# Kernel tuning notes

Measured on AMD Instinct MI355X. Metric: run time of the kernel, lower is better.

The kernel has to match this reference:

```python
import jax, jax.numpy as jnp
import numpy as np

WINDOW_SIZE = 5
CONSISTENCY_WEIGHT = 1.0


def _wsum(x, w):
    # sliding-window sum along axis 1 via exclusive cumsum differences
    s = jnp.cumsum(x, axis=1)
    s = jnp.pad(s, ((0, 0), (1, 0)))
    return s[:, w:] - s[:, :-w]  # [B, L-w+1]


def setup_inputs() -> dict:
    key = jax.random.key(0)
    k1, k2, k3 = jax.random.split(key, 3)
    B, L, C = 512, 16384, 2
    return {
        "predictions": jax.random.normal(k1, (B, L, C), dtype=jnp.float32),
        "targets": jax.random.randint(k2, (B, L), 0, 2, dtype=jnp.int32),
        "mask": jax.random.randint(k3, (B, L), 0, 2, dtype=jnp.int32),
    }


def reference(predictions, targets, mask):
    w = WINDOW_SIZE
    probs = jax.nn.softmax(predictions, axis=-1)[..., 1]  # [B, L]
    t = targets.astype(jnp.float32)
    m = mask.astype(jnp.float32)

    msum = _wsum(m, w)                       # [B, W]
    denom = jnp.maximum(msum, 1.0)           # clamp(min=1.0)
    spm = _wsum(probs * m, w)
    stm = _wsum(t * m, w)
    sp2m = _wsum(probs * probs * m, w)
    st2m = _wsum(t * t * m, w)

    pmean = spm / denom
    tmean = stm / denom
    # masked biased variance: sum((x - mean)^2 * m) / clamp(msum, 1)
    pvar = (sp2m - 2.0 * pmean * spm + pmean * pmean * msum) / denom
    tvar = (st2m - 2.0 * tmean * stm + tmean * tmean * msum) / denom

    mse = jnp.mean((pvar - tvar) ** 2, axis=0)          # per-window MSE over batch, [W]
    valid = (jnp.sum(msum, axis=0) > 0).astype(jnp.float32)  # skip windows with zero mask
    cnt = jnp.maximum(jnp.sum(valid), 1.0)
    loss = jnp.sum(mse * valid) / cnt * CONSISTENCY_WEIGHT
    return loss
```

## Files before the change

### kernel.cpp

```cpp
#include <hip/hip_runtime.h>
#include <math.h>

#define BATCH 512
#define LEN   16384
#define WIN   5
#define WOUT  (LEN - WIN + 1)
#define TPB   256
#define WPT   4
#define WPB   (TPB * WPT)
#define EPT   (WPT + WIN - 1)
#define NCH2  16

__device__ __forceinline__ float fast_rcp(float x) {
    float r = __builtin_amdgcn_rcpf(x);
    return r * fmaf(-x, r, 2.0f);
}

struct RowRaw {
    int4   m0, m1, t0, t1;
    float4 q0, q1, q2, q3;
};

struct RowArr {
    float m[EPT], tm[EPT], pm[EPT], p2m[EPT];
};

__device__ __forceinline__ RowRaw load_row(const float* __restrict__ pred,
                                           const int*   __restrict__ tgt,
                                           const int*   __restrict__ msk,
                                           size_t base) {
    RowRaw r;
    r.m0 = *(const int4*)(msk + base);
    r.m1 = *(const int4*)(msk + base + 4);
    r.t0 = *(const int4*)(tgt + base);
    r.t1 = *(const int4*)(tgt + base + 4);
    r.q0 = *(const float4*)(pred + base * 2);
    r.q1 = *(const float4*)(pred + base * 2 + 4);
    r.q2 = *(const float4*)(pred + base * 2 + 8);
    r.q3 = *(const float4*)(pred + base * 2 + 12);
    return r;
}

__device__ __forceinline__ RowArr convert_row(const RowRaw& r) {
    RowArr a;
    const int mi[EPT] = {r.m0.x, r.m0.y, r.m0.z, r.m0.w,
                         r.m1.x, r.m1.y, r.m1.z, r.m1.w};
    const int ti[EPT] = {r.t0.x, r.t0.y, r.t0.z, r.t0.w,
                         r.t1.x, r.t1.y, r.t1.z, r.t1.w};
    const float dx[EPT] = {r.q0.x - r.q0.y, r.q0.z - r.q0.w,
                           r.q1.x - r.q1.y, r.q1.z - r.q1.w,
                           r.q2.x - r.q2.y, r.q2.z - r.q2.w,
                           r.q3.x - r.q3.y, r.q3.z - r.q3.w};
#pragma unroll
    for (int i = 0; i < EPT; ++i) {
        const float p  = fast_rcp(1.0f + __expf(dx[i]));
        const float mf = (float)mi[i];
        a.m[i]   = mf;
        a.tm[i]  = (float)(ti[i] & mi[i]);
        a.pm[i]  = p * mf;
        a.p2m[i] = p * p * mf;
    }
    return a;
}

__device__ __forceinline__ void windows_row(const RowArr& a,
                                            float accd2[WPT], float accms[WPT]) {
#pragma unroll
    for (int w = 0; w < WPT; ++w) {
        float msum = 0.f, stm = 0.f, spm = 0.f, sp2m = 0.f;
#pragma unroll
        for (int k = 0; k < WIN; ++k) {
            msum += a.m[w + k];
            stm  += a.tm[w + k];
            spm  += a.pm[w + k];
            sp2m += a.p2m[w + k];
        }
        const float denom = fmaxf(msum, 1.0f);
        const float inv   = fast_rcp(denom);
        const float pmean = spm * inv;
        const float tmean = stm * inv;
        const float pvar  = (sp2m - 2.0f * pmean * spm + pmean * pmean * msum) * inv;
        const float tvar  = (stm  - 2.0f * tmean * stm + tmean * tmean * msum) * inv;
        const float d = pvar - tvar;
        accd2[w] += d * d;
        accms[w] += msum;
    }
}

__global__ __launch_bounds__(TPB)
void bcl_partial_kernel(const float* __restrict__ pred,
                        const int*   __restrict__ tgt,
                        const int*   __restrict__ msk,
                        float* __restrict__ part_d2,
                        float* __restrict__ part_ms,
                        int bper) {
    const int j0 = blockIdx.x * WPB + (int)threadIdx.x * WPT;
    if (j0 >= WOUT) return;
    const int b0 = blockIdx.y * bper;

    float accd2[WPT] = {0.f, 0.f, 0.f, 0.f};
    float accms[WPT] = {0.f, 0.f, 0.f, 0.f};

    size_t base = (size_t)b0 * LEN + j0;

    RowRaw raw = load_row(pred, tgt, msk, base);
    RowArr arr = convert_row(raw);

    for (int it = 1; it < bper; ++it) {
        raw = load_row(pred, tgt, msk, base + (size_t)it * LEN);
        windows_row(arr, accd2, accms);
        arr = convert_row(raw);
    }
    windows_row(arr, accd2, accms);

    *(float4*)(part_d2 + (size_t)blockIdx.y * WOUT + j0) =
        make_float4(accd2[0], accd2[1], accd2[2], accd2[3]);
    *(float4*)(part_ms + (size_t)blockIdx.y * WOUT + j0) =
        make_float4(accms[0], accms[1], accms[2], accms[3]);
}

__global__ __launch_bounds__(TPB)
void bcl_chunk_reduce(const float* __restrict__ part_d2,
                      const float* __restrict__ part_ms,
                      float* __restrict__ p2_d2,
                      float* __restrict__ p2_ms,
                      double* __restrict__ accum,
                      unsigned int* __restrict__ ticket,
                      int rf) {
    if (blockIdx.x == 0 && blockIdx.y == 0 && threadIdx.x == 0) {
        accum[0] = 0.0; accum[1] = 0.0; *ticket = 0u;
    }
    const int j = blockIdx.x * blockDim.x + threadIdx.x;
    if (j >= WOUT) return;
    const int c0 = blockIdx.y * rf;
    float d2 = 0.f, ms = 0.f;
#pragma unroll 8
    for (int c = c0; c < c0 + rf; ++c) {
        d2 += part_d2[(size_t)c * WOUT + j];
        ms += part_ms[(size_t)c * WOUT + j];
    }
    p2_d2[(size_t)blockIdx.y * WOUT + j] = d2;
    p2_ms[(size_t)blockIdx.y * WOUT + j] = ms;
}

__global__ __launch_bounds__(TPB)
void bcl_window_reduce(const float* __restrict__ p2_d2,
                       const float* __restrict__ p2_ms,
                       double* __restrict__ accum,
                       unsigned int* __restrict__ ticket,
                       float* __restrict__ out,
                       int nch2) {
    const int j = blockIdx.x * blockDim.x + threadIdx.x;
    double num = 0.0, cnt = 0.0;
    if (j < WOUT) {
        float d2 = 0.f, ms = 0.f;
#pragma unroll 8
        for (int c = 0; c < nch2; ++c) {
            d2 += p2_d2[(size_t)c * WOUT + j];
            ms += p2_ms[(size_t)c * WOUT + j];
        }
        if (ms > 0.f) {
            num = (double)d2 * (1.0 / (double)BATCH);
            cnt = 1.0;
        }
    }
    for (int off = 32; off > 0; off >>= 1) {
        num += __shfl_down(num, off, 64);
        cnt += __shfl_down(cnt, off, 64);
    }
    __shared__ double s_num[4], s_cnt[4];
    const int lane = threadIdx.x & 63, wave = threadIdx.x >> 6;
    if (lane == 0) { s_num[wave] = num; s_cnt[wave] = cnt; }
    __syncthreads();
    if (threadIdx.x == 0) {
        double n = 0.0, c = 0.0;
        const int nw = (int)(blockDim.x >> 6);
        for (int wv = 0; wv < nw; ++wv) { n += s_num[wv]; c += s_cnt[wv]; }
        atomicAdd(&accum[0], n);
        atomicAdd(&accum[1], c);
        __threadfence();
        const unsigned int t = atomicAdd(ticket, 1u);
        if (t == gridDim.x - 1) {
            out[0] = (float)(accum[0] / fmax(accum[1], 1.0));
        }
    }
}

extern "C" void kernel_launch(void* const* d_in, const int* in_sizes, int n_in,
                              void* d_out, int out_size, void* d_ws, size_t ws_size,
                              hipStream_t stream) {
    const float* pred = (const float*)d_in[0];
    const int*   tgt  = (const int*)d_in[1];
    const int*   msk  = (const int*)d_in[2];
    float* out = (float*)d_out;

    int nchunks = 128;
    while (nchunks > 2) {
        size_t need = (size_t)(nchunks + NCH2) * WOUT * 2 * sizeof(float) + 256;
        if (need <= ws_size) break;
        nchunks >>= 1;
    }
    const int bper = BATCH / nchunks;
    const int nch2 = (nchunks >= NCH2) ? NCH2 : nchunks;
    const int rf   = nchunks / nch2;

    float* part_d2 = (float*)d_ws;
    float* part_ms = part_d2 + (size_t)nchunks * WOUT;
    float* p2_d2   = part_ms + (size_t)nchunks * WOUT;
    float* p2_ms   = p2_d2   + (size_t)NCH2 * WOUT;
    size_t off = ((size_t)((char*)(p2_ms + (size_t)NCH2 * WOUT) - (char*)d_ws) + 15) & ~(size_t)15;
    double* accum = (double*)((char*)d_ws + off);
    unsigned int* ticket = (unsigned int*)(accum + 2);

    const int WBLKS = (WOUT + WPB - 1) / WPB;
    dim3 g1(WBLKS, nchunks);
    bcl_partial_kernel<<<g1, TPB, 0, stream>>>(pred, tgt, msk, part_d2, part_ms, bper);

    const int RBLKS = (WOUT + TPB - 1) / TPB;
    dim3 gA(RBLKS, nch2);
    bcl_chunk_reduce<<<gA, TPB, 0, stream>>>(part_d2, part_ms, p2_d2, p2_ms,
                                             accum, ticket, rf);

    bcl_window_reduce<<<RBLKS, TPB, 0, stream>>>(p2_d2, p2_ms, accum, ticket, out, nch2);
}
```

Baseline: 164.7 us.

## Fuse partial and reduction kernels into one cooperative launch with grid sync

Replaces the three-kernel pipeline with a single cooperative kernel that computes per-chunk partial window sums, grid-syncs, reduces over chunks and windows, then grid-syncs again to write the final loss. The chunk count drops from 128 to 64, so each block handles more batch rows, and the manual software prefetch of the next row is removed from the partial loop. The aim is to remove kernel-launch gaps and the intermediate second-level reduction. The trade-offs are grid.sync overhead, fewer blocks in flight, and a fallback path that runs if the cooperative launch fails.

```diff
diff --git a/kernel.cpp b/kernel.cpp
--- a/kernel.cpp
+++ b/kernel.cpp
@@ -1,5 +1,8 @@
 #include <hip/hip_runtime.h>
+#include <hip/hip_cooperative_groups.h>
 #include <math.h>
+
+namespace cg = cooperative_groups;
 
 #define BATCH 512
 #define LEN   16384
@@ -9,6 +12,8 @@
 #define WPT   4
 #define WPB   (TPB * WPT)
 #define EPT   (WPT + WIN - 1)
+#define WBLKS ((WOUT + WPB - 1) / WPB)
+#define RWGS  ((WOUT + TPB - 1) / TPB)
 #define NCH2  16
 
 __device__ __forceinline__ float fast_rcp(float x) {
@@ -20,7 +25,6 @@
     int4   m0, m1, t0, t1;
     float4 q0, q1, q2, q3;
 };
-
 struct RowArr {
     float m[EPT], tm[EPT], pm[EPT], p2m[EPT];
 };
@@ -87,6 +91,91 @@
     }
 }
 
+__device__ __forceinline__ void partial_phase(const float* __restrict__ pred,
+                                              const int*   __restrict__ tgt,
+                                              const int*   __restrict__ msk,
+                                              float* __restrict__ part_d2,
+                                              float* __restrict__ part_ms,
+                                              int col, int chunk, int bper) {
+    const int j0 = col * WPB + (int)threadIdx.x * WPT;
+    if (j0 >= WOUT) return;
+    const int b0 = chunk * bper;
+
+    float accd2[WPT] = {0.f, 0.f, 0.f, 0.f};
+    float accms[WPT] = {0.f, 0.f, 0.f, 0.f};
+
+    size_t base = (size_t)b0 * LEN + j0;
+    for (int it = 0; it < bper; ++it) {
+        RowRaw raw = load_row(pred, tgt, msk, base + (size_t)it * LEN);
+        RowArr arr = convert_row(raw);
+        windows_row(arr, accd2, accms);
+    }
+
+    *(float4*)(part_d2 + (size_t)chunk * WOUT + j0) =
+        make_float4(accd2[0], accd2[1], accd2[2], accd2[3]);
+    *(float4*)(part_ms + (size_t)chunk * WOUT + j0) =
+        make_float4(accms[0], accms[1], accms[2], accms[3]);
+}
+
+__global__ __launch_bounds__(TPB)
+void bcl_fused(const float* __restrict__ pred,
+               const int*   __restrict__ tgt,
+               const int*   __restrict__ msk,
+               float* __restrict__ part_d2,
+               float* __restrict__ part_ms,
+               double* __restrict__ accum,
+               float* __restrict__ out,
+               int nchunks, int bper) {
+    cg::grid_group grid = cg::this_grid();
+    const int wg    = blockIdx.x;
+    const int col   = wg & (WBLKS - 1);
+    const int chunk = wg >> 4;
+
+    if (wg == 0 && threadIdx.x == 0) { accum[0] = 0.0; accum[1] = 0.0; }
+
+    partial_phase(pred, tgt, msk, part_d2, part_ms, col, chunk, bper);
+
+    grid.sync();
+
+    if (wg < RWGS) {
+        const int j = wg * TPB + (int)threadIdx.x;
+        double num = 0.0, cnt = 0.0;
+        if (j < WOUT) {
+            float d2 = 0.f, ms = 0.f;
+#pragma unroll 8
+            for (int c = 0; c < nchunks; ++c) {
+                d2 += part_d2[(size_t)c * WOUT + j];
+                ms += part_ms[(size_t)c * WOUT + j];
+            }
+            if (ms > 0.f) {
+                num = (double)d2 * (1.0 / (double)BATCH);
+                cnt = 1.0;
+            }
+        }
+        for (int off = 32; off > 0; off >>= 1) {
+            num += __shfl_down(num, off, 64);
+            cnt += __shfl_down(cnt, off, 64);
+        }
+        __shared__ double s_num[4], s_cnt[4];
+        const int lane = threadIdx.x & 63, wave = threadIdx.x >> 6;
+        if (lane == 0) { s_num[wave] = num; s_cnt[wave] = cnt; }
+        __syncthreads();
+        if (threadIdx.x == 0) {
+            double n = 0.0, c = 0.0;
+            for (int wv = 0; wv < TPB / 64; ++wv) { n += s_num[wv]; c += s_cnt[wv]; }
+            atomicAdd(&accum[0], n);
+            atomicAdd(&accum[1], c);
+            __threadfence();
+        }
+    }
+
+    grid.sync();
+
+    if (wg == 0 && threadIdx.x == 0) {
+        out[0] = (float)(accum[0] / fmax(accum[1], 1.0));
+    }
+}
+
 __global__ __launch_bounds__(TPB)
 void bcl_partial_kernel(const float* __restrict__ pred,
                         const int*   __restrict__ tgt,
@@ -94,29 +183,7 @@
                         float* __restrict__ part_d2,
                         float* __restrict__ part_ms,
                         int bper) {
-    const int j0 = blockIdx.x * WPB + (int)threadIdx.x * WPT;
-    if (j0 >= WOUT) return;
-    const int b0 = blockIdx.y * bper;
-
-    float accd2[WPT] = {0.f, 0.f, 0.f, 0.f};
-    float accms[WPT] = {0.f, 0.f, 0.f, 0.f};
-
-    size_t base = (size_t)b0 * LEN + j0;
-
-    RowRaw raw = load_row(pred, tgt, msk, base);
-    RowArr arr = convert_row(raw);
-
-    for (int it = 1; it < bper; ++it) {
-        raw = load_row(pred, tgt, msk, base + (size_t)it * LEN);
-        windows_row(arr, accd2, accms);
-        arr = convert_row(raw);
-    }
-    windows_row(arr, accd2, accms);
-
-    *(float4*)(part_d2 + (size_t)blockIdx.y * WOUT + j0) =
-        make_float4(accd2[0], accd2[1], accd2[2], accd2[3]);
-    *(float4*)(part_ms + (size_t)blockIdx.y * WOUT + j0) =
-        make_float4(accms[0], accms[1], accms[2], accms[3]);
+    partial_phase(pred, tgt, msk, part_d2, part_ms, blockIdx.x, blockIdx.y, bper);
 }
 
 __global__ __launch_bounds__(TPB)
@@ -174,8 +241,7 @@
     __syncthreads();
     if (threadIdx.x == 0) {
         double n = 0.0, c = 0.0;
-        const int nw = (int)(blockDim.x >> 6);
-        for (int wv = 0; wv < nw; ++wv) { n += s_num[wv]; c += s_cnt[wv]; }
+        for (int wv = 0; wv < TPB / 64; ++wv) { n += s_num[wv]; c += s_cnt[wv]; }
         atomicAdd(&accum[0], n);
         atomicAdd(&accum[1], c);
         __threadfence();
@@ -194,15 +260,13 @@
     const int*   msk  = (const int*)d_in[2];
     float* out = (float*)d_out;
 
-    int nchunks = 128;
+    int nchunks = 64;
     while (nchunks > 2) {
         size_t need = (size_t)(nchunks + NCH2) * WOUT * 2 * sizeof(float) + 256;
         if (need <= ws_size) break;
         nchunks >>= 1;
     }
     const int bper = BATCH / nchunks;
-    const int nch2 = (nchunks >= NCH2) ? NCH2 : nchunks;
-    const int rf   = nchunks / nch2;
 
     float* part_d2 = (float*)d_ws;
     float* part_ms = part_d2 + (size_t)nchunks * WOUT;
@@ -212,14 +276,22 @@
     double* accum = (double*)((char*)d_ws + off);
     unsigned int* ticket = (unsigned int*)(accum + 2);
 
-    const int WBLKS = (WOUT + WPB - 1) / WPB;
+    dim3 gF(WBLKS * nchunks);
+    int nck = nchunks, bp = bper;
+    void* args[] = { (void*)&pred, (void*)&tgt, (void*)&msk,
+                     (void*)&part_d2, (void*)&part_ms,
+                     (void*)&accum, (void*)&out, (void*)&nck, (void*)&bp };
+    hipError_t e = hipLaunchCooperativeKernel((const void*)bcl_fused, gF, dim3(TPB),
+                                              args, 0, stream);
+    if (e == hipSuccess) return;
+    (void)hipGetLastError();
+
+    const int nch2 = (nchunks >= NCH2) ? NCH2 : nchunks;
+    const int rf   = nchunks / nch2;
     dim3 g1(WBLKS, nchunks);
     bcl_partial_kernel<<<g1, TPB, 0, stream>>>(pred, tgt, msk, part_d2, part_ms, bper);
-
-    const int RBLKS = (WOUT + TPB - 1) / TPB;
-    dim3 gA(RBLKS, nch2);
+    dim3 gA(RWGS, nch2);
     bcl_chunk_reduce<<<gA, TPB, 0, stream>>>(part_d2, part_ms, p2_d2, p2_ms,
                                              accum, ticket, rf);
-
-    bcl_window_reduce<<<RBLKS, TPB, 0, stream>>>(p2_d2, p2_ms, accum, ticket, out, nch2);
-}
+    bcl_window_reduce<<<RWGS, TPB, 0, stream>>>(p2_d2, p2_ms, accum, ticket, out, nch2);
+}
```

Result: slower. 389.7 us (+136.6%).

## Stage row tiles into LDS with async global_load_lds double buffering

Applied to the files above, without the earlier changes.

The partial kernel no longer has each thread issue overlapping vector loads straight from global memory. Each workgroup now copies its mask, target and prediction tile for a batch row into LDS with async global-to-LDS loads, using two buffers so the next row is fetched while the current one is computed. The goal is to cut redundant halo traffic and hide load latency. In exchange it adds a vmcnt wait and a block barrier per row, uses about 38 KB of LDS per workgroup (which can limit occupancy), and clamps source offsets at the row end.

```diff
diff --git a/kernel.cpp b/kernel.cpp
--- a/kernel.cpp
+++ b/kernel.cpp
@@ -9,7 +9,14 @@
 #define WPT   4
 #define WPB   (TPB * WPT)
 #define EPT   (WPT + WIN - 1)
+#define WBLKS ((WOUT + WPB - 1) / WPB)
+#define RWGS  ((WOUT + TPB - 1) / TPB)
 #define NCH2  16
+
+#define LBUF   19456
+#define MT_ISS 5
+#define PR_ISS 9
+#define N_ISS  (2 * MT_ISS + PR_ISS)
 
 __device__ __forceinline__ float fast_rcp(float x) {
     float r = __builtin_amdgcn_rcpf(x);
@@ -20,26 +27,9 @@
     int4   m0, m1, t0, t1;
     float4 q0, q1, q2, q3;
 };
-
 struct RowArr {
     float m[EPT], tm[EPT], pm[EPT], p2m[EPT];
 };
-
-__device__ __forceinline__ RowRaw load_row(const float* __restrict__ pred,
-                                           const int*   __restrict__ tgt,
-                                           const int*   __restrict__ msk,
-                                           size_t base) {
-    RowRaw r;
-    r.m0 = *(const int4*)(msk + base);
-    r.m1 = *(const int4*)(msk + base + 4);
-    r.t0 = *(const int4*)(tgt + base);
-    r.t1 = *(const int4*)(tgt + base + 4);
-    r.q0 = *(const float4*)(pred + base * 2);
-    r.q1 = *(const float4*)(pred + base * 2 + 4);
-    r.q2 = *(const float4*)(pred + base * 2 + 8);
-    r.q3 = *(const float4*)(pred + base * 2 + 12);
-    return r;
-}
 
 __device__ __forceinline__ RowArr convert_row(const RowRaw& r) {
     RowArr a;
@@ -88,35 +78,94 @@
 }
 
 __global__ __launch_bounds__(TPB)
-void bcl_partial_kernel(const float* __restrict__ pred,
+void bcl_partial_staged(const float* __restrict__ pred,
                         const int*   __restrict__ tgt,
                         const int*   __restrict__ msk,
                         float* __restrict__ part_d2,
                         float* __restrict__ part_ms,
                         int bper) {
-    const int j0 = blockIdx.x * WPB + (int)threadIdx.x * WPT;
-    if (j0 >= WOUT) return;
-    const int b0 = blockIdx.y * bper;
+    __shared__ __align__(1024) char s_lds[2 * LBUF];
+    const int col   = blockIdx.x;
+    const int chunk = blockIdx.y;
+    const int tid   = (int)threadIdx.x;
+    const int lane  = tid & 63, wid = tid >> 6;
+    const int j0    = col * WPB + tid * WPT;
+    const int b0    = chunk * bper;
+
+    const char* mbytes = (const char*)msk;
+    const char* tbytes = (const char*)tgt;
+    const char* pbytes = (const char*)pred;
+    const int cmt = col * (WPB * 4);
+    const int cpr = col * (WPB * 8);
+
+    auto stage = [&](char* buf, int b) {
+        const char* mrow = mbytes + (size_t)b * (LEN * 4);
+        const char* trow = tbytes + (size_t)b * (LEN * 4);
+        const char* prow = pbytes + (size_t)b * (LEN * 8);
+        for (int i = wid; i < N_ISS; i += 4) {
+            const char* src; char* dst;
+            if (i < MT_ISS) {
+                int off = cmt + (i << 10);
+                if (off > LEN * 4 - 1024) off = LEN * 4 - 1024;
+                src = mrow + off;  dst = buf + (i << 10);
+            } else if (i < 2 * MT_ISS) {
+                const int k = i - MT_ISS;
+                int off = cmt + (k << 10);
+                if (off > LEN * 4 - 1024) off = LEN * 4 - 1024;
+                src = trow + off;  dst = buf + 5120 + (k << 10);
+            } else {
+                const int k = i - 2 * MT_ISS;
+                int off = cpr + (k << 10);
+                if (off > LEN * 8 - 1024) off = LEN * 8 - 1024;
+                src = prow + off;  dst = buf + 10240 + (k << 10);
+            }
+            __builtin_amdgcn_global_load_lds(
+                (const __attribute__((address_space(1))) unsigned int*)(src + lane * 16),
+                (__attribute__((address_space(3))) unsigned int*)dst,
+                16, 0, 0);
+        }
+    };
+
+    char* cur = s_lds;
+    char* nxt = s_lds + LBUF;
 
     float accd2[WPT] = {0.f, 0.f, 0.f, 0.f};
     float accms[WPT] = {0.f, 0.f, 0.f, 0.f};
 
-    size_t base = (size_t)b0 * LEN + j0;
-
-    RowRaw raw = load_row(pred, tgt, msk, base);
-    RowArr arr = convert_row(raw);
-
-    for (int it = 1; it < bper; ++it) {
-        raw = load_row(pred, tgt, msk, base + (size_t)it * LEN);
-        windows_row(arr, accd2, accms);
-        arr = convert_row(raw);
-    }
-    windows_row(arr, accd2, accms);
-
-    *(float4*)(part_d2 + (size_t)blockIdx.y * WOUT + j0) =
-        make_float4(accd2[0], accd2[1], accd2[2], accd2[3]);
-    *(float4*)(part_ms + (size_t)blockIdx.y * WOUT + j0) =
-        make_float4(accms[0], accms[1], accms[2], accms[3]);
+    stage(cur, b0);
+    asm volatile("s_waitcnt vmcnt(0)" ::: "memory");
+    __syncthreads();
+
+    for (int it = 0; it < bper; ++it) {
+        if (it + 1 < bper) stage(nxt, b0 + it + 1);
+
+        if (j0 < WOUT) {
+            RowRaw r;
+            const int e0 = tid << 4;
+            r.m0 = *(const int4*)(cur + e0);
+            r.m1 = *(const int4*)(cur + e0 + 16);
+            r.t0 = *(const int4*)(cur + 5120 + e0);
+            r.t1 = *(const int4*)(cur + 5120 + e0 + 16);
+            const int p0 = 10240 + (tid << 5);
+            r.q0 = *(const float4*)(cur + p0);
+            r.q1 = *(const float4*)(cur + p0 + 16);
+            r.q2 = *(const float4*)(cur + p0 + 32);
+            r.q3 = *(const float4*)(cur + p0 + 48);
+            RowArr a = convert_row(r);
+            windows_row(a, accd2, accms);
+        }
+
+        asm volatile("s_waitcnt vmcnt(0)" ::: "memory");
+        __syncthreads();
+        char* t = cur; cur = nxt; nxt = t;
+    }
+
+    if (j0 < WOUT) {
+        *(float4*)(part_d2 + (size_t)chunk * WOUT + j0) =
+            make_float4(accd2[0], accd2[1], accd2[2], accd2[3]);
+        *(float4*)(part_ms + (size_t)chunk * WOUT + j0) =
+            make_float4(accms[0], accms[1], accms[2], accms[3]);
+    }
 }
 
 __global__ __launch_bounds__(TPB)
@@ -174,8 +223,7 @@
     __syncthreads();
     if (threadIdx.x == 0) {
         double n = 0.0, c = 0.0;
-        const int nw = (int)(blockDim.x >> 6);
-        for (int wv = 0; wv < nw; ++wv) { n += s_num[wv]; c += s_cnt[wv]; }
+        for (int wv = 0; wv < TPB / 64; ++wv) { n += s_num[wv]; c += s_cnt[wv]; }
         atomicAdd(&accum[0], n);
         atomicAdd(&accum[1], c);
         __threadfence();
@@ -212,14 +260,12 @@
     double* accum = (double*)((char*)d_ws + off);
     unsigned int* ticket = (unsigned int*)(accum + 2);
 
-    const int WBLKS = (WOUT + WPB - 1) / WPB;
     dim3 g1(WBLKS, nchunks);
-    bcl_partial_kernel<<<g1, TPB, 0, stream>>>(pred, tgt, msk, part_d2, part_ms, bper);
-
-    const int RBLKS = (WOUT + TPB - 1) / TPB;
-    dim3 gA(RBLKS, nch2);
+    bcl_partial_staged<<<g1, TPB, 0, stream>>>(pred, tgt, msk, part_d2, part_ms, bper);
+
+    dim3 gA(RWGS, nch2);
     bcl_chunk_reduce<<<gA, TPB, 0, stream>>>(part_d2, part_ms, p2_d2, p2_ms,
                                              accum, ticket, rf);
 
-    bcl_window_reduce<<<RBLKS, TPB, 0, stream>>>(p2_d2, p2_ms, accum, ticket, out, nch2);
-}
+    bcl_window_reduce<<<RWGS, TPB, 0, stream>>>(p2_d2, p2_ms, accum, ticket, out, nch2);
+}
```

Result: no change. 167.2 us (+1.5%).
